# Kernel optimization log

Measured on AMD Instinct MI355X. Metric: run time of the kernel, lower is better.

## Reference

```python
import jax, jax.numpy as jnp
import numpy as np

N_HEAD = 16
N_KV_HEAD = 8
HEAD_DIM = 64
EPS_NORM = 1e-6


def _rms_norm(x):
    # F.rms_norm without learned weight
    return x * jax.lax.rsqrt(jnp.mean(x * x, axis=-1, keepdims=True) + EPS_NORM)


def _apply_rotary_emb(x, cos, sin):
    # x: [B, T, H, D]; cos/sin: [T, 1, D/2] (broadcast over B and H)
    d = x.shape[-1] // 2
    x1, x2 = x[..., :d], x[..., d:]
    return jnp.concatenate([x1 * cos + x2 * sin, -x1 * sin + x2 * cos], axis=-1)


def setup_inputs() -> dict:
    key = jax.random.key(0)
    ks = jax.random.split(key, 8)
    B, T, C = 2, 2048, 1024
    return {
        "x": jax.random.normal(ks[0], (B, T, C), jnp.float32),
        "cos": jax.random.uniform(ks[1], (T, 1, HEAD_DIM // 2), jnp.float32),
        "sin": jax.random.uniform(ks[2], (T, 1, HEAD_DIM // 2), jnp.float32),
        "Wq": jax.random.normal(ks[3], (N_HEAD * HEAD_DIM, C), jnp.float32) * 0.02,
        "Wk": jax.random.normal(ks[4], (N_KV_HEAD * HEAD_DIM, C), jnp.float32) * 0.02,
        "Wv": jax.random.normal(ks[5], (N_KV_HEAD * HEAD_DIM, C), jnp.float32) * 0.02,
        "Wproj": jax.random.normal(ks[6], (C, C), jnp.float32) * 0.02,
        "w_braid": jax.random.normal(ks[7], (HEAD_DIM,), jnp.float32),
    }


def reference(x, cos, sin, Wq, Wk, Wv, Wproj, w_braid):
    B, T, C = x.shape
    q = (x @ Wq.T).reshape(B, T, N_HEAD, HEAD_DIM)
    k = (x @ Wk.T).reshape(B, T, N_KV_HEAD, HEAD_DIM)
    v = (x @ Wv.T).reshape(B, T, N_KV_HEAD, HEAD_DIM)
    q = _rms_norm(_apply_rotary_emb(q, cos, sin))
    k = _rms_norm(_apply_rotary_emb(k, cos, sin))
    # [B, H, T, D]
    q = q.transpose(0, 2, 1, 3)
    k = k.transpose(0, 2, 1, 3)
    v = v.transpose(0, 2, 1, 3)
    rep = N_HEAD // N_KV_HEAD
    k = jnp.repeat(k, rep, axis=1)  # GQA repeat_kv_heads
    v = jnp.repeat(v, rep, axis=1)
    # rank-1 outer-sum score: s_q[i] + s_k[j]
    s_q = jnp.einsum("bhtd,d->bht", q, w_braid)
    s_k = jnp.einsum("bhsd,d->bhs", k, w_braid)
    scores = s_q[..., :, None] + s_k[..., None, :]  # [B, H, T, T]
    causal = jnp.arange(T)[:, None] >= jnp.arange(T)[None, :]
    scores = jnp.where(causal, scores, -jnp.inf)
    attn = jax.nn.sigmoid(scores)  # non-softmax gating
    y = jnp.einsum("bhts,bhsd->bhtd", attn, v)
    y = y / (T ** 0.5 + 1e-6)
    y = y.transpose(0, 2, 1, 3).reshape(B, T, C)
    return y @ Wproj.T
```

## Files before the change

kernel.cpp:

```cpp
#include <hip/hip_runtime.h>
#include <math.h>

#define BATCH   2
#define T_LEN   2048
#define C_DIM   1024
#define NH      16
#define NKV     8
#define HD      64

typedef unsigned short u16;
typedef __attribute__((ext_vector_type(8))) short short8;
typedef __attribute__((ext_vector_type(4))) float floatx4;

__device__ __forceinline__ u16 f2bf(float f) {
    union { float f; unsigned u; } v; v.f = f;
    unsigned r = v.u + 0x7FFF + ((v.u >> 16) & 1);
    return (u16)(r >> 16);
}

__device__ __forceinline__ void gload_lds16(const u16* g, u16* l) {
    __builtin_amdgcn_global_load_lds(
        (const __attribute__((address_space(1))) void*)g,
        (__attribute__((address_space(3))) void*)l, 16, 0, 0);
}

__global__ __launch_bounds__(256)
void cvt_all(const float* __restrict__ x, const float* __restrict__ Wq,
             const float* __restrict__ Wk, const float* __restrict__ Wv,
             const float* __restrict__ Wp, u16* __restrict__ xb,
             u16* __restrict__ Wqkvb, u16* __restrict__ Wpb) {
    const int blk = blockIdx.x;
    const float* src; u16* dst; long off;
    if (blk < 4096)      { src = x;  dst = xb;              off = (long)blk * 1024; }
    else if (blk < 5120) { src = Wq; dst = Wqkvb;           off = (long)(blk - 4096) * 1024; }
    else if (blk < 5632) { src = Wk; dst = Wqkvb + 1048576; off = (long)(blk - 5120) * 1024; }
    else if (blk < 6144) { src = Wv; dst = Wqkvb + 1572864; off = (long)(blk - 5632) * 1024; }
    else                 { src = Wp; dst = Wpb;             off = (long)(blk - 6144) * 1024; }
    const float* s = src + (off - off % 1024);
    (void)s;
    long i = (long)threadIdx.x * 4;
    float4 f = *(const float4*)&src[off % (1 << 30) == off ? off + i : off + i];
    f = *(const float4*)&src[off + i];
    ushort4 o;
    o.x = f2bf(f.x); o.y = f2bf(f.y); o.z = f2bf(f.z); o.w = f2bf(f.w);
    *(ushort4*)&dst[off + i] = o;
}

__global__ __launch_bounds__(256)
void gemm_bf16_nt(const u16* __restrict__ A, const u16* __restrict__ B,
                  float* __restrict__ C, int M, int N, int K) {
    __shared__ u16 As[128 * 32];
    __shared__ u16 Bs[128 * 32];
    const int tid    = threadIdx.x;
    const int lane   = tid & 63;
    const int wave   = tid >> 6;
    const int row_in = lane & 15;
    const int quad   = lane >> 4;
    const int koff   = quad * 8;
    const int rw     = (wave & 1) * 64;
    const int cw     = (wave >> 1) * 64;
    const int row0   = blockIdx.y * 128;
    const int col0   = blockIdx.x * 128;

    floatx4 acc[4][4] = {};

    for (int k0 = 0; k0 < K; k0 += 32) {
        #pragma unroll
        for (int c = 0; c < 2; ++c) {
            const int l  = c * 256 + tid;
            const int r  = l >> 2;
            const int kc = l & 3;
            gload_lds16(A + (size_t)(row0 + r) * K + k0 + kc * 8, &As[(size_t)l * 8]);
            gload_lds16(B + (size_t)(col0 + r) * K + k0 + kc * 8, &Bs[(size_t)l * 8]);
        }
        __syncthreads();
        short8 af[4], bf_[4];
        #pragma unroll
        for (int i = 0; i < 4; ++i)
            af[i] = *(const short8*)&As[(rw + 16 * i + row_in) * 32 + koff];
        #pragma unroll
        for (int j = 0; j < 4; ++j)
            bf_[j] = *(const short8*)&Bs[(cw + 16 * j + row_in) * 32 + koff];
        #pragma unroll
        for (int i = 0; i < 4; ++i)
            #pragma unroll
            for (int j = 0; j < 4; ++j)
                acc[i][j] = __builtin_amdgcn_mfma_f32_16x16x32_bf16(af[i], bf_[j], acc[i][j], 0, 0, 0);
        __syncthreads();
    }

    #pragma unroll
    for (int i = 0; i < 4; ++i)
        #pragma unroll
        for (int j = 0; j < 4; ++j)
            #pragma unroll
            for (int r = 0; r < 4; ++r)
                C[(size_t)(row0 + rw + 16 * i + quad * 4 + r) * N + col0 + cw + 16 * j + row_in]
                    = acc[i][j][r];
}

__global__ __launch_bounds__(256)
void gemm_bf16_nt2(const u16* __restrict__ A, const u16* __restrict__ B,
                   float* __restrict__ C, int M, int N, int K) {
    __shared__ u16 As[128 * 32];
    __shared__ u16 Bs[64 * 32];
    const int tid    = threadIdx.x;
    const int lane   = tid & 63;
    const int wave   = tid >> 6;
    const int row_in = lane & 15;
    const int quad   = lane >> 4;
    const int koff   = quad * 8;
    const int rw     = (wave & 1) * 64;
    const int cw     = (wave >> 1) * 32;
    const int row0   = blockIdx.y * 128;
    const int col0   = blockIdx.x * 64;

    floatx4 acc[4][2] = {};

    for (int k0 = 0; k0 < K; k0 += 32) {
        #pragma unroll
        for (int c = 0; c < 2; ++c) {
            const int l  = c * 256 + tid;
            const int r  = l >> 2;
            const int kc = l & 3;
            gload_lds16(A + (size_t)(row0 + r) * K + k0 + kc * 8, &As[(size_t)l * 8]);
        }
        {
            const int r  = tid >> 2;
            const int kc = tid & 3;
            gload_lds16(B + (size_t)(col0 + r) * K + k0 + kc * 8, &Bs[(size_t)tid * 8]);
        }
        __syncthreads();
        short8 af[4], bf_[2];
        #pragma unroll
        for (int i = 0; i < 4; ++i)
            af[i] = *(const short8*)&As[(rw + 16 * i + row_in) * 32 + koff];
        #pragma unroll
        for (int j = 0; j < 2; ++j)
            bf_[j] = *(const short8*)&Bs[(cw + 16 * j + row_in) * 32 + koff];
        #pragma unroll
        for (int i = 0; i < 4; ++i)
            #pragma unroll
            for (int j = 0; j < 2; ++j)
                acc[i][j] = __builtin_amdgcn_mfma_f32_16x16x32_bf16(af[i], bf_[j], acc[i][j], 0, 0, 0);
        __syncthreads();
    }

    #pragma unroll
    for (int i = 0; i < 4; ++i)
        #pragma unroll
        for (int j = 0; j < 2; ++j)
            #pragma unroll
            for (int r = 0; r < 4; ++r)
                C[(size_t)(row0 + rw + 16 * i + quad * 4 + r) * N + col0 + cw + 16 * j + row_in]
                    = acc[i][j][r];
}

__global__ __launch_bounds__(256)
void rope_norm_dot(const float* __restrict__ qkv, const float* __restrict__ cosb,
                   const float* __restrict__ sinb, const float* __restrict__ wb,
                   float* __restrict__ sq, float* __restrict__ sk) {
    const int wave = threadIdx.x >> 6;
    const int lane = threadIdx.x & 63;
    const long vec = (long)blockIdx.x * 4 + wave;
    const float* src; float* dst; int t;
    if (vec < 65536) {
        const int h = (int)(vec & 15);
        const long bt = vec >> 4;
        t = (int)(bt & 2047);
        const int b = (int)(bt >> 11);
        src = qkv + bt * 2048 + h * 64;
        dst = sq + ((long)b * NH + h) * T_LEN + t;
    } else {
        const long vk = vec - 65536;
        const int h = (int)(vk & 7);
        const long bt = vk >> 3;
        t = (int)(bt & 2047);
        const int b = (int)(bt >> 11);
        src = qkv + bt * 2048 + 1024 + h * 64;
        dst = sk + ((long)b * NKV + h) * T_LEN + t;
    }

    const int j = lane & 31;
    const float x1 = src[j];
    const float x2 = src[j + 32];
    const float c  = cosb[t * 32 + j];
    const float s  = sinb[t * 32 + j];
    float r = (lane < 32) ? fmaf(x1, c, x2 * s) : fmaf(x2, c, -x1 * s);

    float ss = r * r;
    #pragma unroll
    for (int m = 1; m < 64; m <<= 1) ss += __shfl_xor(ss, m, 64);
    const float scale = rsqrtf(ss * (1.0f / 64.0f) + 1e-6f);

    float dt = r * scale * wb[lane];
    #pragma unroll
    for (int m = 1; m < 64; m <<= 1) dt += __shfl_xor(dt, m, 64);
    if (lane == 0)
        *dst = fminf(fmaxf(dt, -44.0f), 44.0f);
}

__global__ __launch_bounds__(256)
void vt_convert(const float* __restrict__ qkv, u16* __restrict__ Vt) {
    __shared__ float L[64][65];
    const int t0  = blockIdx.x * 64;
    const int bkv = blockIdx.y;
    const int b   = bkv >> 3;
    const int kvh = bkv & 7;
    const int tid = threadIdx.x;
    const float* src = qkv + ((size_t)b * T_LEN + t0) * 2048 + 1536 + kvh * 64;
    #pragma unroll
    for (int l = 0; l < 16; ++l) {
        int idx = tid + l * 256;
        int s = idx >> 6, d = idx & 63;
        L[s][d] = src[(size_t)s * 2048 + d];
    }
    __syncthreads();
    u16* dst = Vt + (size_t)bkv * 64 * T_LEN + t0;
    #pragma unroll
    for (int l = 0; l < 16; ++l) {
        int idx = tid + l * 256;
        int d = idx >> 6, s = idx & 63;
        dst[(size_t)d * T_LEN + s] = f2bf(L[s][d]);
    }
}

__global__ __launch_bounds__(512)
void braid_attn(const float* __restrict__ sq, const float* __restrict__ sk,
                const u16* __restrict__ Vt, u16* __restrict__ yb) {
    __shared__ u16 Vd[2][4096];
    __shared__ float eskl[128];
    float* red = (float*)&Vd[0][0];

    const int bh   = blockIdx.y;
    const int b    = bh >> 4;
    const int h    = bh & 15;
    const int p    = blockIdx.x;
    const int tid  = threadIdx.x;
    const int lane = tid & 63;
    const int wave = tid >> 6;
    const int sg   = wave >> 2;
    const int w4   = wave & 3;
    const int n    = lane & 15;
    const int quad = lane >> 4;
    const int row  = w4 * 16 + n;

    const float* sq_p = sq + (size_t)bh * T_LEN;
    const float* sk_p = sk + ((size_t)b * NKV + (h >> 1)) * T_LEN;
    const u16*   vt_b = Vt + ((size_t)b * NKV + (h >> 1)) * 64 * T_LEN;
    const float  inv  = (float)(1.0 / (45.254833995939045 + 1e-6));

    for (int ph = 0; ph < 2; ++ph) {
        const int t0 = (ph ? p : (31 - p)) * 64;
        const float a = __expf(-sq_p[t0 + row]);
        const int send = t0 + 64;
        floatx4 acc[4] = {};

        for (int s0 = 0; s0 < send; s0 += 128) {
            __syncthreads();
            {
                const int r = tid >> 3, g = tid & 7;
                const int so = (g ^ (r & 7)) << 3;
                gload_lds16(vt_b + (size_t)r * T_LEN + s0 + so, &Vd[0][(size_t)tid * 8]);
                if (s0 + 64 < send)
                    gload_lds16(vt_b + (size_t)r * T_LEN + s0 + 64 + so, &Vd[1][(size_t)tid * 8]);
            }
            if (tid < 128 && (tid < 64 || s0 + 64 < send))
                eskl[tid] = __expf(-sk_p[s0 + tid]);
            __syncthreads();

            const int s0g = s0 + sg * 64;
            if (s0g < send) {
                const bool diag = (s0g == t0);
                #pragma unroll
                for (int kk = 0; kk < 2; ++kk) {
                    const float* eb = &eskl[sg * 64 + kk * 32 + quad * 8];
                    const float4 e0 = *(const float4*)eb;
                    const float4 e1 = *(const float4*)(eb + 4);
                    const float ev[8] = {e0.x, e0.y, e0.z, e0.w, e1.x, e1.y, e1.z, e1.w};
                    union { unsigned u[4]; short8 s8; } af;
                    #pragma unroll
                    for (int jj = 0; jj < 4; ++jj) {
                        float r0 = __builtin_amdgcn_rcpf(fmaf(ev[2 * jj],     a, 1.0f));
                        float r1 = __builtin_amdgcn_rcpf(fmaf(ev[2 * jj + 1], a, 1.0f));
                        if (diag) {
                            const int s_ = kk * 32 + quad * 8 + 2 * jj;
                            if (s_     > row) r0 = 0.0f;
                            if (s_ + 1 > row) r1 = 0.0f;
                        }
                        af.u[jj] = __builtin_amdgcn_perm(__float_as_uint(r1),
                                                         __float_as_uint(r0), 0x07060302u);
                    }
                    #pragma unroll
                    for (int j = 0; j < 4; ++j) {
                        const short8 bfr = *(const short8*)
                            &Vd[sg][(16 * j + n) * 64 + (((kk * 4 + quad) ^ (n & 7)) << 3)];
                        acc[j] = __builtin_amdgcn_mfma_f32_16x16x32_bf16(af.s8, bfr, acc[j], 0, 0, 0);
                    }
                }
            }
        }

        __syncthreads();
        if (sg == 1) {
            #pragma unroll
            for (int j = 0; j < 4; ++j)
                #pragma unroll
                for (int r = 0; r < 4; ++r)
                    red[(j * 4 + r) * 256 + w4 * 64 + lane] = acc[j][r];
        }
        __syncthreads();
        if (sg == 0) {
            #pragma unroll
            for (int j = 0; j < 4; ++j)
                #pragma unroll
                for (int r = 0; r < 4; ++r) {
                    const float o = acc[j][r] + red[(j * 4 + r) * 256 + w4 * 64 + lane];
                    const int t = t0 + w4 * 16 + quad * 4 + r;
                    yb[((size_t)b * T_LEN + t) * C_DIM + h * HD + 16 * j + n] = f2bf(o * inv);
                }
        }
    }
}

extern "C" void kernel_launch(void* const* d_in, const int* in_sizes, int n_in,
                              void* d_out, int out_size, void* d_ws, size_t ws_size,
                              hipStream_t stream) {
    const float* x     = (const float*)d_in[0];
    const float* cosb  = (const float*)d_in[1];
    const float* sinb  = (const float*)d_in[2];
    const float* Wq    = (const float*)d_in[3];
    const float* Wk    = (const float*)d_in[4];
    const float* Wv    = (const float*)d_in[5];
    const float* Wproj = (const float*)d_in[6];
    const float* wb    = (const float*)d_in[7];
    float* out = (float*)d_out;

    char* w = (char*)d_ws;
    u16* xb     = (u16*)w;  w += (size_t)4096 * 1024 * 2;
    u16* Wqkvb  = (u16*)w;  w += (size_t)2048 * 1024 * 2;
    u16* Wpb    = (u16*)w;  w += (size_t)1024 * 1024 * 2;
    u16* yb     = (u16*)w;  w += (size_t)4096 * 1024 * 2;
    u16* VtB    = (u16*)w;  w += (size_t)BATCH * NKV * 64 * T_LEN * 2;
    float* qkv  = (float*)w; w += (size_t)4096 * 2048 * 4;
    float* sq   = (float*)w; w += (size_t)BATCH * NH * T_LEN * 4;
    float* sk   = (float*)w; w += (size_t)BATCH * NKV * T_LEN * 4;

    dim3 blk(256);
    cvt_all<<<7168, blk, 0, stream>>>(x, Wq, Wk, Wv, Wproj, xb, Wqkvb, Wpb);
    gemm_bf16_nt<<<dim3(16, 32), blk, 0, stream>>>(xb, Wqkvb, qkv, 4096, 2048, 1024);
    rope_norm_dot<<<24576, blk, 0, stream>>>(qkv, cosb, sinb, wb, sq, sk);
    vt_convert<<<dim3(32, 16), blk, 0, stream>>>(qkv, VtB);
    braid_attn<<<dim3(16, 32), dim3(512), 0, stream>>>(sq, sk, VtB, yb);
    gemm_bf16_nt2<<<dim3(16, 32), blk, 0, stream>>>(yb, Wpb, out, 4096, 1024, 1024);
}
```

Baseline: 183.9 us.

## Store QKV projection in bf16 and fuse rope/norm with V transpose kernel

The QKV GEMM now writes bf16 instead of fp32, halving the intermediate's write and read traffic. The rope/norm/dot kernel and the V-transpose kernel are merged into one launch that reads bf16 with vector loads. The exp of the score terms is moved out of the attention loop into this producer. Rounding q/k to bf16 before rope and rms-norm adds some numerical error.

```diff
diff --git a/kernel.cpp b/kernel.cpp
--- a/kernel.cpp
+++ b/kernel.cpp
@@ -1,5 +1,4 @@
 #include <hip/hip_runtime.h>
-#include <math.h>
 
 #define BATCH   2
 #define T_LEN   2048
@@ -16,6 +15,11 @@
     union { float f; unsigned u; } v; v.f = f;
     unsigned r = v.u + 0x7FFF + ((v.u >> 16) & 1);
     return (u16)(r >> 16);
+}
+
+__device__ __forceinline__ float bf2f(u16 b) {
+    union { unsigned u; float f; } v; v.u = ((unsigned)b) << 16;
+    return v.f;
 }
 
 __device__ __forceinline__ void gload_lds16(const u16* g, u16* l) {
@@ -36,19 +40,16 @@
     else if (blk < 5632) { src = Wk; dst = Wqkvb + 1048576; off = (long)(blk - 5120) * 1024; }
     else if (blk < 6144) { src = Wv; dst = Wqkvb + 1572864; off = (long)(blk - 5632) * 1024; }
     else                 { src = Wp; dst = Wpb;             off = (long)(blk - 6144) * 1024; }
-    const float* s = src + (off - off % 1024);
-    (void)s;
-    long i = (long)threadIdx.x * 4;
-    float4 f = *(const float4*)&src[off % (1 << 30) == off ? off + i : off + i];
-    f = *(const float4*)&src[off + i];
+    const long i = off + (long)threadIdx.x * 4;
+    const float4 f = *(const float4*)&src[i];
     ushort4 o;
     o.x = f2bf(f.x); o.y = f2bf(f.y); o.z = f2bf(f.z); o.w = f2bf(f.w);
-    *(ushort4*)&dst[off + i] = o;
+    *(ushort4*)&dst[i] = o;
 }
 
 __global__ __launch_bounds__(256)
-void gemm_bf16_nt(const u16* __restrict__ A, const u16* __restrict__ B,
-                  float* __restrict__ C, int M, int N, int K) {
+void gemm_bf16_nt_b16(const u16* __restrict__ A, const u16* __restrict__ B,
+                      u16* __restrict__ C, int M, int N, int K) {
     __shared__ u16 As[128 * 32];
     __shared__ u16 Bs[128 * 32];
     const int tid    = threadIdx.x;
@@ -96,8 +97,8 @@
             #pragma unroll
             for (int r = 0; r < 4; ++r)
                 C[(size_t)(row0 + rw + 16 * i + quad * 4 + r) * N + col0 + cw + 16 * j + row_in]
-                    = acc[i][j][r];
-}
+                    = f2bf(acc[i][j][r]);
+    }
 
 __global__ __launch_bounds__(256)
 void gemm_bf16_nt2(const u16* __restrict__ A, const u16* __restrict__ B,
@@ -157,36 +158,69 @@
 }
 
 __global__ __launch_bounds__(256)
-void rope_norm_dot(const float* __restrict__ qkv, const float* __restrict__ cosb,
-                   const float* __restrict__ sinb, const float* __restrict__ wb,
-                   float* __restrict__ sq, float* __restrict__ sk) {
-    const int wave = threadIdx.x >> 6;
-    const int lane = threadIdx.x & 63;
-    const long vec = (long)blockIdx.x * 4 + wave;
-    const float* src; float* dst; int t;
+void post_qkv(const u16* __restrict__ qkvb, const float* __restrict__ cosb,
+              const float* __restrict__ sinb, const float* __restrict__ wb,
+              float* __restrict__ esq, float* __restrict__ esk,
+              u16* __restrict__ Vt) {
+    __shared__ u16 Lu[64][72];
+    const int blk = blockIdx.x;
+    const int tid = threadIdx.x;
+
+    if (blk < 512) {
+        const int bkv = blk >> 5;
+        const int t0  = (blk & 31) * 64;
+        const int b   = bkv >> 3;
+        const int kvh = bkv & 7;
+        const u16* src = qkvb + ((size_t)b * T_LEN + t0) * 2048 + 1536 + kvh * 64;
+        #pragma unroll
+        for (int c = 0; c < 2; ++c) {
+            const int i = c * 256 + tid;
+            const int s = i >> 3, d0 = (i & 7) * 8;
+            *(short8*)&Lu[s][d0] = *(const short8*)&src[(size_t)s * 2048 + d0];
+        }
+        __syncthreads();
+        u16* dst = Vt + (size_t)bkv * 64 * T_LEN + t0;
+        #pragma unroll
+        for (int c = 0; c < 2; ++c) {
+            const int i = c * 256 + tid;
+            const int d = i >> 3, s0 = (i & 7) * 8;
+            short8 o;
+            #pragma unroll
+            for (int j = 0; j < 8; ++j) o[j] = (short)Lu[s0 + j][d];
+            *(short8*)&dst[(size_t)d * T_LEN + s0] = o;
+        }
+        return;
+    }
+
+    const int wave = tid >> 6;
+    const int lane = tid & 63;
+    const long vec = (long)(blk - 512) * 4 + wave;
+    const u16* src; float* dst; int t;
     if (vec < 65536) {
         const int h = (int)(vec & 15);
         const long bt = vec >> 4;
         t = (int)(bt & 2047);
         const int b = (int)(bt >> 11);
-        src = qkv + bt * 2048 + h * 64;
-        dst = sq + ((long)b * NH + h) * T_LEN + t;
+        src = qkvb + bt * 2048 + h * 64;
+        dst = esq + ((long)b * NH + h) * T_LEN + t;
     } else {
         const long vk = vec - 65536;
         const int h = (int)(vk & 7);
         const long bt = vk >> 3;
         t = (int)(bt & 2047);
         const int b = (int)(bt >> 11);
-        src = qkv + bt * 2048 + 1024 + h * 64;
-        dst = sk + ((long)b * NKV + h) * T_LEN + t;
-    }
-
+        src = qkvb + bt * 2048 + 1024 + h * 64;
+        dst = esk + ((long)b * NKV + h) * T_LEN + t;
+    }
+
+    const float v  = bf2f(src[lane]);
+    const float ot = __shfl_xor(v, 32, 64);
     const int j = lane & 31;
-    const float x1 = src[j];
-    const float x2 = src[j + 32];
+    const float x1 = (lane < 32) ? v : ot;
+    const float x2 = (lane < 32) ? ot : v;
     const float c  = cosb[t * 32 + j];
     const float s  = sinb[t * 32 + j];
-    float r = (lane < 32) ? fmaf(x1, c, x2 * s) : fmaf(x2, c, -x1 * s);
+    const float r  = (lane < 32) ? fmaf(x1, c, x2 * s) : fmaf(x2, c, -x1 * s);
 
     float ss = r * r;
     #pragma unroll
@@ -197,36 +231,11 @@
     #pragma unroll
     for (int m = 1; m < 64; m <<= 1) dt += __shfl_xor(dt, m, 64);
     if (lane == 0)
-        *dst = fminf(fmaxf(dt, -44.0f), 44.0f);
-}
-
-__global__ __launch_bounds__(256)
-void vt_convert(const float* __restrict__ qkv, u16* __restrict__ Vt) {
-    __shared__ float L[64][65];
-    const int t0  = blockIdx.x * 64;
-    const int bkv = blockIdx.y;
-    const int b   = bkv >> 3;
-    const int kvh = bkv & 7;
-    const int tid = threadIdx.x;
-    const float* src = qkv + ((size_t)b * T_LEN + t0) * 2048 + 1536 + kvh * 64;
-    #pragma unroll
-    for (int l = 0; l < 16; ++l) {
-        int idx = tid + l * 256;
-        int s = idx >> 6, d = idx & 63;
-        L[s][d] = src[(size_t)s * 2048 + d];
-    }
-    __syncthreads();
-    u16* dst = Vt + (size_t)bkv * 64 * T_LEN + t0;
-    #pragma unroll
-    for (int l = 0; l < 16; ++l) {
-        int idx = tid + l * 256;
-        int d = idx >> 6, s = idx & 63;
-        dst[(size_t)d * T_LEN + s] = f2bf(L[s][d]);
-    }
+        *dst = __expf(-fminf(fmaxf(dt, -44.0f), 44.0f));
 }
 
 __global__ __launch_bounds__(512)
-void braid_attn(const float* __restrict__ sq, const float* __restrict__ sk,
+void braid_attn(const float* __restrict__ esq, const float* __restrict__ esk,
                 const u16* __restrict__ Vt, u16* __restrict__ yb) {
     __shared__ u16 Vd[2][4096];
     __shared__ float eskl[128];
@@ -245,14 +254,14 @@
     const int quad = lane >> 4;
     const int row  = w4 * 16 + n;
 
-    const float* sq_p = sq + (size_t)bh * T_LEN;
-    const float* sk_p = sk + ((size_t)b * NKV + (h >> 1)) * T_LEN;
-    const u16*   vt_b = Vt + ((size_t)b * NKV + (h >> 1)) * 64 * T_LEN;
-    const float  inv  = (float)(1.0 / (45.254833995939045 + 1e-6));
+    const float* esq_p = esq + (size_t)bh * T_LEN;
+    const float* esk_p = esk + ((size_t)b * NKV + (h >> 1)) * T_LEN;
+    const u16*   vt_b  = Vt + ((size_t)b * NKV + (h >> 1)) * 64 * T_LEN;
+    const float  inv   = (float)(1.0 / (45.254833995939045 + 1e-6));
 
     for (int ph = 0; ph < 2; ++ph) {
         const int t0 = (ph ? p : (31 - p)) * 64;
-        const float a = __expf(-sq_p[t0 + row]);
+        const float a = esq_p[t0 + row];
         const int send = t0 + 64;
         floatx4 acc[4] = {};
 
@@ -266,7 +275,7 @@
                     gload_lds16(vt_b + (size_t)r * T_LEN + s0 + 64 + so, &Vd[1][(size_t)tid * 8]);
             }
             if (tid < 128 && (tid < 64 || s0 + 64 < send))
-                eskl[tid] = __expf(-sk_p[s0 + tid]);
+                eskl[tid] = esk_p[s0 + tid];
             __syncthreads();
 
             const int s0g = s0 + sg * 64;
@@ -340,17 +349,16 @@
     u16* xb     = (u16*)w;  w += (size_t)4096 * 1024 * 2;
     u16* Wqkvb  = (u16*)w;  w += (size_t)2048 * 1024 * 2;
     u16* Wpb    = (u16*)w;  w += (size_t)1024 * 1024 * 2;
+    u16* qkvb   = (u16*)w;  w += (size_t)4096 * 2048 * 2;
     u16* yb     = (u16*)w;  w += (size_t)4096 * 1024 * 2;
     u16* VtB    = (u16*)w;  w += (size_t)BATCH * NKV * 64 * T_LEN * 2;
-    float* qkv  = (float*)w; w += (size_t)4096 * 2048 * 4;
-    float* sq   = (float*)w; w += (size_t)BATCH * NH * T_LEN * 4;
-    float* sk   = (float*)w; w += (size_t)BATCH * NKV * T_LEN * 4;
+    float* esq  = (float*)w; w += (size_t)BATCH * NH * T_LEN * 4;
+    float* esk  = (float*)w; w += (size_t)BATCH * NKV * T_LEN * 4;
 
     dim3 blk(256);
     cvt_all<<<7168, blk, 0, stream>>>(x, Wq, Wk, Wv, Wproj, xb, Wqkvb, Wpb);
-    gemm_bf16_nt<<<dim3(16, 32), blk, 0, stream>>>(xb, Wqkvb, qkv, 4096, 2048, 1024);
-    rope_norm_dot<<<24576, blk, 0, stream>>>(qkv, cosb, sinb, wb, sq, sk);
-    vt_convert<<<dim3(32, 16), blk, 0, stream>>>(qkv, VtB);
-    braid_attn<<<dim3(16, 32), dim3(512), 0, stream>>>(sq, sk, VtB, yb);
+    gemm_bf16_nt_b16<<<dim3(16, 32), blk, 0, stream>>>(xb, Wqkvb, qkvb, 4096, 2048, 1024);
+    post_qkv<<<512 + 24576, blk, 0, stream>>>(qkvb, cosb, sinb, wb, esq, esk, VtB);
+    braid_attn<<<dim3(16, 32), dim3(512), 0, stream>>>(esq, esk, VtB, yb);
     gemm_bf16_nt2<<<dim3(16, 32), blk, 0, stream>>>(yb, Wpb, out, 4096, 1024, 1024);
 }
```

Measured after the change: 180.2 us. 1.02x faster.
